# Kernel tuning notes

Hardware: AMD Instinct MI355X
Metric: run time of the kernel (lower is better)

Reference implementation:

```python
import jax, jax.numpy as jnp
import numpy as np

B, T, H, W = 64, 128, 64, 64
K = 3          # conv kernel size
NH = 64        # hidden_dim == n_qubits (required for the gating math to broadcast)
IN = 1         # input_dim (scalar conv feature per frame)
NC = 10        # num_classes


def setup_inputs() -> dict:
    key = jax.random.key(0)
    ks = jax.random.split(key, 32)
    i = iter(range(32))

    def lin(kw, kb, fan_in, fan_out):
        s = 1.0 / np.sqrt(fan_in)
        w = jax.random.uniform(kw, (fan_out, fan_in), jnp.float32, -s, s)
        b = jax.random.uniform(kb, (fan_out,), jnp.float32, -s, s)
        return w, b

    inp = {"images": jax.random.normal(ks[next(i)], (B, T, 1, H, W), jnp.float32)}
    inp["threshold"] = jnp.float32(0.5)
    s = 1.0 / np.sqrt(K * K)
    inp["conv_w"] = jax.random.uniform(ks[next(i)], (1, 1, K, K), jnp.float32, -s, s)
    inp["conv_b"] = jax.random.uniform(ks[next(i)], (1,), jnp.float32, -s, s)
    for g in ("f", "i", "u", "o"):
        w, b = lin(ks[next(i)], ks[next(i)], IN + NH, NH)
        inp[f"fc_{g}_w"], inp[f"fc_{g}_b"] = w, b
        lw, lb = lin(ks[next(i)], ks[next(i)], NH, NH)
        ew, eb = lin(ks[next(i)], ks[next(i)], NH, NH)
        inp[f"q_{g}_lw"], inp[f"q_{g}_lb"] = lw, lb
        inp[f"q_{g}_ew"], inp[f"q_{g}_eb"] = ew, eb
    inp["cls_w"], inp["cls_b"] = lin(ks[next(i)], ks[next(i)], NH, NC)
    return inp


def _qlayer(x, lw, lb, ew, eb):
    out = jnp.tanh(x @ lw.T + lb)
    return out * jax.nn.sigmoid(out @ ew.T + eb)


def reference(images, threshold, conv_w, conv_b,
              fc_f_w, fc_f_b, fc_i_w, fc_i_b, fc_u_w, fc_u_b, fc_o_w, fc_o_b,
              q_f_lw, q_f_lb, q_f_ew, q_f_eb,
              q_i_lw, q_i_lb, q_i_ew, q_i_eb,
              q_u_lw, q_u_lb, q_u_ew, q_u_eb,
              q_o_lw, q_o_lb, q_o_ew, q_o_eb,
              cls_w, cls_b):
    b, t, c, h, w = images.shape
    nh = q_f_lw.shape[0]
    # ConvFilter over all frames at once (vectorized across batch*time)
    x = images.reshape(b * t, c, h, w)
    logits = jax.lax.conv_general_dilated(
        x, conv_w, (1, 1), "VALID",
        dimension_numbers=("NCHW", "OIHW", "NCHW")) + conv_b[None, :, None, None]
    feat = jax.nn.sigmoid(logits - threshold).mean(axis=(2, 3))  # [B*T, 1]
    seq = feat.reshape(b, t, 1).transpose(1, 0, 2)               # [T, B, 1]

    def step(carry, xt):
        hx, cx = carry
        comb = jnp.concatenate([xt, hx], axis=1)                 # [B, 1+NH]
        f = jax.nn.sigmoid(_qlayer(comb @ fc_f_w.T + fc_f_b, q_f_lw, q_f_lb, q_f_ew, q_f_eb))
        i = jax.nn.sigmoid(_qlayer(comb @ fc_i_w.T + fc_i_b, q_i_lw, q_i_lb, q_i_ew, q_i_eb))
        g = jnp.tanh(_qlayer(comb @ fc_u_w.T + fc_u_b, q_u_lw, q_u_lb, q_u_ew, q_u_eb))
        o = jax.nn.sigmoid(_qlayer(comb @ fc_o_w.T + fc_o_b, q_o_lw, q_o_lb, q_o_ew, q_o_eb))
        cx = f * cx + i * g
        hx = o * jnp.tanh(cx)
        return (hx, cx), hx

    h0 = jnp.zeros((b, nh), images.dtype)
    c0 = jnp.zeros((b, nh), images.dtype)
    _, outs = jax.lax.scan(step, (h0, c0), seq)                  # [T, B, NH]
    return outs @ cls_w.T + cls_b                                # [T, B, NC]
```

## Files before the change

### kernel.cpp

```cpp
#include <hip/hip_runtime.h>

#define T_ 128
#define B_ 64
#define NH_ 64
#define NC_ 10

__device__ __forceinline__ float sigmoid_f(float x) {
    return 1.0f / (1.0f + __expf(-x));
}
__device__ __forceinline__ float tanh_f(float x) {
    return 1.0f - 2.0f / (1.0f + __expf(2.0f * x));
}
__device__ __forceinline__ void dot4(const float4 a, const float4 v,
                                     float& p0, float& p1, float& p2, float& p3) {
    p0 = fmaf(a.x, v.x, p0);
    p1 = fmaf(a.y, v.y, p1);
    p2 = fmaf(a.z, v.z, p2);
    p3 = fmaf(a.w, v.w, p3);
}

#define IMP 68
__global__ __launch_bounds__(256) void conv_feat(const float* __restrict__ img,
                                                 const float* __restrict__ cw,
                                                 const float* __restrict__ cb,
                                                 const float* __restrict__ thr,
                                                 float* __restrict__ feat) {
    __shared__ __align__(16) float im[64 * IMP];
    __shared__ float wsum[4];
    const int tid = threadIdx.x;
    const float* src = img + (size_t)blockIdx.x * 4096;
#pragma unroll
    for (int i = 0; i < 4; i++) {
        const int idx = i * 256 + tid;
        const int row = idx >> 4, c4 = idx & 15;
        *(float4*)&im[row * IMP + c4 * 4] = *(const float4*)&src[idx * 4];
    }
    const float w0 = cw[0], w1 = cw[1], w2 = cw[2], w3 = cw[3], w4 = cw[4],
                w5 = cw[5], w6 = cw[6], w7 = cw[7], w8 = cw[8];
    const float bias = cb[0] - thr[0];
    __syncthreads();

    const int r  = tid >> 2;
    const int c0 = (tid & 3) * 16;
    float sum = 0.0f;
    if (r < 62) {
        const int ncols = (c0 == 48) ? 14 : 16;
        float acc[16];
#pragma unroll
        for (int x = 0; x < 16; x++) acc[x] = bias;
#pragma unroll
        for (int dr = 0; dr < 3; dr++) {
            float rb[20];
#pragma unroll
            for (int j = 0; j < 5; j++) {
                float4 v = *(const float4*)&im[(r + dr) * IMP + c0 + j * 4];
                rb[j * 4 + 0] = v.x; rb[j * 4 + 1] = v.y;
                rb[j * 4 + 2] = v.z; rb[j * 4 + 3] = v.w;
            }
            const float k0 = (dr == 0) ? w0 : (dr == 1) ? w3 : w6;
            const float k1 = (dr == 0) ? w1 : (dr == 1) ? w4 : w7;
            const float k2 = (dr == 0) ? w2 : (dr == 1) ? w5 : w8;
#pragma unroll
            for (int x = 0; x < 16; x++) {
                acc[x] = fmaf(rb[x], k0, acc[x]);
                acc[x] = fmaf(rb[x + 1], k1, acc[x]);
                acc[x] = fmaf(rb[x + 2], k2, acc[x]);
            }
        }
#pragma unroll
        for (int x = 0; x < 16; x++)
            if (x < ncols) sum += sigmoid_f(acc[x]);
    }
#pragma unroll
    for (int off = 32; off >= 1; off >>= 1) sum += __shfl_down(sum, off, 64);
    const int wv = tid >> 6, ln = tid & 63;
    if (ln == 0) wsum[wv] = sum;
    __syncthreads();
    if (tid == 0)
        feat[blockIdx.x] = (wsum[0] + wsum[1] + wsum[2] + wsum[3]) * (1.0f / 3844.0f);
}

struct FuseArgs {
    const float* fcw[4];
    const float* fcb[4];
    const float* lw[4];
    const float* lb[4];
};

__global__ __launch_bounds__(256) void fuse_kernel(FuseArgs a, float* __restrict__ Aall,
                                                   float* __restrict__ Vall,
                                                   float* __restrict__ Call) {
    const int g = blockIdx.x;
    const float* fcw = a.fcw[g];
    const float* fcb = a.fcb[g];
    const float* lw  = a.lw[g];
    const float* lb  = a.lb[g];
    __shared__ float fcs[64 * 65];
    __shared__ float fbs[64];
    for (int i = threadIdx.x; i < 64 * 65; i += 256) fcs[i] = fcw[i];
    if (threadIdx.x < 64) fbs[threadIdx.x] = fcb[threadIdx.x];
    __syncthreads();

    const int n = threadIdx.x >> 2;
    const int j0 = (threadIdx.x & 3) * 16;
    float lrow[64];
#pragma unroll
    for (int k = 0; k < 64; k++) lrow[k] = lw[n * 64 + k];

    for (int j = j0; j < j0 + 16; j++) {
        float s = 0.0f;
#pragma unroll
        for (int k = 0; k < 64; k++) s = fmaf(lrow[k], fcs[k * 65 + j + 1], s);
        Aall[(g * 64 + n) * 64 + j] = s;
    }
    if ((threadIdx.x & 3) == 0) {
        float sv = 0.0f, sc = 0.0f;
#pragma unroll
        for (int k = 0; k < 64; k++) {
            sv = fmaf(lrow[k], fcs[k * 65], sv);
            sc = fmaf(lrow[k], fbs[k], sc);
        }
        Vall[g * 64 + n] = sv;
        Call[g * 64 + n] = sc + lb[n];
    }
}

__global__ __launch_bounds__(512, 1) void recur(
    const float* __restrict__ feat, const float* __restrict__ Aall,
    const float* __restrict__ Vall, const float* __restrict__ Call,
    const float* __restrict__ ew_f, const float* __restrict__ eb_f,
    const float* __restrict__ ew_i, const float* __restrict__ eb_i,
    const float* __restrict__ ew_u, const float* __restrict__ eb_u,
    const float* __restrict__ ew_o, const float* __restrict__ eb_o,
    const float* __restrict__ cls_w, const float* __restrict__ cls_b,
    float* __restrict__ out) {
    const int b = blockIdx.x;
    const int tid = threadIdx.x;
    const int wave = tid >> 6;
    const int g = wave >> 1;
    const int nh = wave & 1;
    const int lane = tid & 63;
    const int s = lane >> 5;
    const int n = nh * 32 + (lane & 31);
    const int gn = g * 64 + n;
    const float* ew  = (g == 0) ? ew_f : (g == 1) ? ew_i : (g == 2) ? ew_u : ew_o;
    const float* ebp = (g == 0) ? eb_f : (g == 1) ? eb_i : (g == 2) ? eb_u : eb_o;

    const float4* ap = (const float4*)&Aall[gn * 64 + s * 32];
    const float4* ep = (const float4*)&ew[n * 64 + s * 32];
    const float4 wa0 = ap[0], wa1 = ap[1], wa2 = ap[2], wa3 = ap[3];
    const float4 wa4 = ap[4], wa5 = ap[5], wa6 = ap[6], wa7 = ap[7];
    const float4 we0 = ep[0], we1 = ep[1], we2 = ep[2], we3 = ep[3];
    const float4 we4 = ep[4], we5 = ep[5], we6 = ep[6], we7 = ep[7];
    const float vj = Vall[gn], cj = Call[gn], ebj = ebp[n];

    __shared__ __align__(16) float hx[64];
    __shared__ __align__(16) float qsh[4][64];
    __shared__ __align__(16) float acts[2][4][64];
    __shared__ __align__(16) float xts[T_];
    __shared__ float hist[T_ * 65];
    __shared__ float cwts[NC_ * 65 + NC_];

    for (int i = tid; i < T_; i += 512) xts[i] = feat[b * T_ + i];
    for (int i = tid; i < NC_ * 64; i += 512) {
        int c = i >> 6, k = i & 63;
        cwts[c * 65 + k] = cls_w[i];
    }
    if (tid < NC_) cwts[NC_ * 65 + tid] = cls_b[tid];
    if (tid < 64) hx[tid] = 0.0f;
    float cx = 0.0f;
    __syncthreads();

    const float4* hp = (const float4*)&hx[s * 32];
    const float4* qp = (const float4*)&qsh[g][s * 32];

    for (int t = 0; t < T_; t++) {
        const float xt = xts[t];

        float p0 = 0, p1 = 0, p2 = 0, p3 = 0;
        {
            float4 v0 = hp[0], v1 = hp[1], v2 = hp[2], v3 = hp[3];
            float4 v4 = hp[4], v5 = hp[5], v6 = hp[6], v7 = hp[7];
            dot4(wa0, v0, p0, p1, p2, p3);
            dot4(wa1, v1, p0, p1, p2, p3);
            dot4(wa2, v2, p0, p1, p2, p3);
            dot4(wa3, v3, p0, p1, p2, p3);
            dot4(wa4, v4, p0, p1, p2, p3);
            dot4(wa5, v5, p0, p1, p2, p3);
            dot4(wa6, v6, p0, p1, p2, p3);
            dot4(wa7, v7, p0, p1, p2, p3);
        }
        float p = (p0 + p1) + (p2 + p3);
        p += __shfl_xor(p, 32, 64);
        const float q = tanh_f(fmaf(xt, vj, cj) + p);
        if (s == 0) qsh[g][n] = q;
        __syncthreads();

        p0 = 0; p1 = 0; p2 = 0; p3 = 0;
        {
            float4 v0 = qp[0], v1 = qp[1], v2 = qp[2], v3 = qp[3];
            float4 v4 = qp[4], v5 = qp[5], v6 = qp[6], v7 = qp[7];
            dot4(we0, v0, p0, p1, p2, p3);
            dot4(we1, v1, p0, p1, p2, p3);
            dot4(we2, v2, p0, p1, p2, p3);
            dot4(we3, v3, p0, p1, p2, p3);
            dot4(we4, v4, p0, p1, p2, p3);
            dot4(we5, v5, p0, p1, p2, p3);
            dot4(we6, v6, p0, p1, p2, p3);
            dot4(we7, v7, p0, p1, p2, p3);
        }
        p = (p0 + p1) + (p2 + p3);
        p += __shfl_xor(p, 32, 64);
        const float z = q * sigmoid_f(p + ebj);
        const float act = (g == 2) ? tanh_f(z) : sigmoid_f(z);
        if (s == 0) acts[t & 1][g][n] = act;
        __syncthreads();

        const float ff = acts[t & 1][0][n];
        const float ii = acts[t & 1][1][n];
        const float uu = acts[t & 1][2][n];
        const float oo = acts[t & 1][3][n];
        cx = fmaf(ff, cx, ii * uu);
        const float h = oo * tanh_f(cx);
        if (wave < 2 && s == 0) {
            hx[n] = h;
            hist[t * 65 + n] = h;
        }
        __syncthreads();
    }

#pragma unroll
    for (int j = 0; j < 3; j++) {
        const int o = j * 512 + tid;
        if (o < T_ * NC_) {
            const int r = o / 10;
            const int c = o - r * 10;
            float sacc = cwts[NC_ * 65 + c];
#pragma unroll 16
            for (int k = 0; k < 64; k++)
                sacc = fmaf(hist[r * 65 + k], cwts[c * 65 + k], sacc);
            out[((size_t)r * B_ + b) * NC_ + c] = sacc;
        }
    }
}

extern "C" void kernel_launch(void* const* d_in, const int* in_sizes, int n_in,
                              void* d_out, int out_size, void* d_ws, size_t ws_size,
                              hipStream_t stream) {
    const float* images = (const float*)d_in[0];
    const float* thr    = (const float*)d_in[1];
    const float* convw  = (const float*)d_in[2];
    const float* convb  = (const float*)d_in[3];
    const float* fcw[4]; const float* fcb[4]; const float* lw[4]; const float* lb[4];
    const float* ew[4];  const float* eb[4];
    for (int g = 0; g < 4; g++) {
        int base = 4 + g * 6;
        fcw[g] = (const float*)d_in[base + 0];
        fcb[g] = (const float*)d_in[base + 1];
        lw[g]  = (const float*)d_in[base + 2];
        lb[g]  = (const float*)d_in[base + 3];
        ew[g]  = (const float*)d_in[base + 4];
        eb[g]  = (const float*)d_in[base + 5];
    }
    const float* clsw = (const float*)d_in[28];
    const float* clsb = (const float*)d_in[29];

    float* ws   = (float*)d_ws;
    float* feat = ws;
    float* Aall = ws + 8192;
    float* Vall = ws + 24576;
    float* Call = ws + 24832;

    conv_feat<<<8192, 256, 0, stream>>>(images, convw, convb, thr, feat);

    FuseArgs fa;
    for (int g = 0; g < 4; g++) {
        fa.fcw[g] = fcw[g]; fa.fcb[g] = fcb[g];
        fa.lw[g] = lw[g];   fa.lb[g] = lb[g];
    }
    fuse_kernel<<<4, 256, 0, stream>>>(fa, Aall, Vall, Call);

    recur<<<B_, 512, 0, stream>>>(feat, Aall, Vall, Call,
                                  ew[0], eb[0], ew[1], eb[1],
                                  ew[2], eb[2], ew[3], eb[3],
                                  clsw, clsb, (float*)d_out);
}
```

Before: 163.5 us.

## Keep hidden state in registers and broadcast via ds_swizzle, dropping per-step barrier

Every wave now recomputes the full cell update in its own registers. Each lane owns one hidden unit, and the hidden vector reaches the first matvec through 32 ds_swizzle broadcasts. This removes the shared hx buffer and one of the three __syncthreads per timestep, cutting barrier latency on the serial recurrence's critical path. In exchange, the 8 vector LDS reads become 32 swizzle ops per step, and the cell math is repeated across all waves.

```diff
diff --git a/kernel.cpp b/kernel.cpp
--- a/kernel.cpp
+++ b/kernel.cpp
@@ -18,6 +18,10 @@
     p2 = fmaf(a.z, v.z, p2);
     p3 = fmaf(a.w, v.w, p3);
 }
+
+#define SWZF(J, WW, PP) { \
+    int swz_ = __builtin_amdgcn_ds_swizzle(h_bits, (J) << 5); \
+    PP = fmaf((WW), __int_as_float(swz_), PP); }
 
 #define IMP 68
 __global__ __launch_bounds__(256) void conv_feat(const float* __restrict__ img,
@@ -142,6 +146,7 @@
     const int lane = tid & 63;
     const int s = lane >> 5;
     const int n = nh * 32 + (lane & 31);
+    const int np = s * 32 + (lane & 31);
     const int gn = g * 64 + n;
     const float* ew  = (g == 0) ? ew_f : (g == 1) ? ew_i : (g == 2) ? ew_u : ew_o;
     const float* ebp = (g == 0) ? eb_f : (g == 1) ? eb_i : (g == 2) ? eb_u : eb_o;
@@ -154,7 +159,6 @@
     const float4 we4 = ep[4], we5 = ep[5], we6 = ep[6], we7 = ep[7];
     const float vj = Vall[gn], cj = Call[gn], ebj = ebp[n];
 
-    __shared__ __align__(16) float hx[64];
     __shared__ __align__(16) float qsh[4][64];
     __shared__ __align__(16) float acts[2][4][64];
     __shared__ __align__(16) float xts[T_];
@@ -167,29 +171,24 @@
         cwts[c * 65 + k] = cls_w[i];
     }
     if (tid < NC_) cwts[NC_ * 65 + tid] = cls_b[tid];
-    if (tid < 64) hx[tid] = 0.0f;
-    float cx = 0.0f;
-    __syncthreads();
-
-    const float4* hp = (const float4*)&hx[s * 32];
+    float cx = 0.0f, h_own = 0.0f;
+    __syncthreads();
+
     const float4* qp = (const float4*)&qsh[g][s * 32];
 
     for (int t = 0; t < T_; t++) {
         const float xt = xts[t];
 
+        const int h_bits = __float_as_int(h_own);
         float p0 = 0, p1 = 0, p2 = 0, p3 = 0;
-        {
-            float4 v0 = hp[0], v1 = hp[1], v2 = hp[2], v3 = hp[3];
-            float4 v4 = hp[4], v5 = hp[5], v6 = hp[6], v7 = hp[7];
-            dot4(wa0, v0, p0, p1, p2, p3);
-            dot4(wa1, v1, p0, p1, p2, p3);
-            dot4(wa2, v2, p0, p1, p2, p3);
-            dot4(wa3, v3, p0, p1, p2, p3);
-            dot4(wa4, v4, p0, p1, p2, p3);
-            dot4(wa5, v5, p0, p1, p2, p3);
-            dot4(wa6, v6, p0, p1, p2, p3);
-            dot4(wa7, v7, p0, p1, p2, p3);
-        }
+        SWZF(0,  wa0.x, p0) SWZF(1,  wa0.y, p1) SWZF(2,  wa0.z, p2) SWZF(3,  wa0.w, p3)
+        SWZF(4,  wa1.x, p0) SWZF(5,  wa1.y, p1) SWZF(6,  wa1.z, p2) SWZF(7,  wa1.w, p3)
+        SWZF(8,  wa2.x, p0) SWZF(9,  wa2.y, p1) SWZF(10, wa2.z, p2) SWZF(11, wa2.w, p3)
+        SWZF(12, wa3.x, p0) SWZF(13, wa3.y, p1) SWZF(14, wa3.z, p2) SWZF(15, wa3.w, p3)
+        SWZF(16, wa4.x, p0) SWZF(17, wa4.y, p1) SWZF(18, wa4.z, p2) SWZF(19, wa4.w, p3)
+        SWZF(20, wa5.x, p0) SWZF(21, wa5.y, p1) SWZF(22, wa5.z, p2) SWZF(23, wa5.w, p3)
+        SWZF(24, wa6.x, p0) SWZF(25, wa6.y, p1) SWZF(26, wa6.z, p2) SWZF(27, wa6.w, p3)
+        SWZF(28, wa7.x, p0) SWZF(29, wa7.y, p1) SWZF(30, wa7.z, p2) SWZF(31, wa7.w, p3)
         float p = (p0 + p1) + (p2 + p3);
         p += __shfl_xor(p, 32, 64);
         const float q = tanh_f(fmaf(xt, vj, cj) + p);
@@ -216,18 +215,15 @@
         if (s == 0) acts[t & 1][g][n] = act;
         __syncthreads();
 
-        const float ff = acts[t & 1][0][n];
-        const float ii = acts[t & 1][1][n];
-        const float uu = acts[t & 1][2][n];
-        const float oo = acts[t & 1][3][n];
+        const float ff = acts[t & 1][0][np];
+        const float ii = acts[t & 1][1][np];
+        const float uu = acts[t & 1][2][np];
+        const float oo = acts[t & 1][3][np];
         cx = fmaf(ff, cx, ii * uu);
-        const float h = oo * tanh_f(cx);
-        if (wave < 2 && s == 0) {
-            hx[n] = h;
-            hist[t * 65 + n] = h;
-        }
-        __syncthreads();
-    }
+        h_own = oo * tanh_f(cx);
+        if (wave == 0) hist[t * 65 + np] = h_own;
+    }
+    __syncthreads();
 
 #pragma unroll
     for (int j = 0; j < 3; j++) {
```

Measured after the change: 180.0 us. 1.1x slower.

## Drop per-step barrier in recurrence via per-wave hidden state; batch conv frames

Applied to the files above, without the earlier changes.

In the recurrence, every wave now redundantly computes the full 64-element cell/hidden update into its own private copy of the hidden state. This removes the second block-wide barrier per timestep, at the cost of duplicated elementwise work and extra shared memory. The conv kernel now processes four frames per block. It prefetches the next frame into registers while computing the current one, which cuts block count and overlaps global loads with compute.

```diff
diff --git a/kernel.cpp b/kernel.cpp
--- a/kernel.cpp
+++ b/kernel.cpp
@@ -20,6 +20,7 @@
 }
 
 #define IMP 68
+#define FPB 4
 __global__ __launch_bounds__(256) void conv_feat(const float* __restrict__ img,
                                                  const float* __restrict__ cw,
                                                  const float* __restrict__ cb,
@@ -28,56 +29,73 @@
     __shared__ __align__(16) float im[64 * IMP];
     __shared__ float wsum[4];
     const int tid = threadIdx.x;
-    const float* src = img + (size_t)blockIdx.x * 4096;
-#pragma unroll
-    for (int i = 0; i < 4; i++) {
-        const int idx = i * 256 + tid;
-        const int row = idx >> 4, c4 = idx & 15;
-        *(float4*)&im[row * IMP + c4 * 4] = *(const float4*)&src[idx * 4];
-    }
+    const float* base = img + (size_t)blockIdx.x * FPB * 4096;
     const float w0 = cw[0], w1 = cw[1], w2 = cw[2], w3 = cw[3], w4 = cw[4],
                 w5 = cw[5], w6 = cw[6], w7 = cw[7], w8 = cw[8];
     const float bias = cb[0] - thr[0];
-    __syncthreads();
-
+
+    const int rr = tid >> 4;
+    const int cc = (tid & 15) * 4;
     const int r  = tid >> 2;
     const int c0 = (tid & 3) * 16;
-    float sum = 0.0f;
-    if (r < 62) {
-        const int ncols = (c0 == 48) ? 14 : 16;
-        float acc[16];
-#pragma unroll
-        for (int x = 0; x < 16; x++) acc[x] = bias;
-#pragma unroll
-        for (int dr = 0; dr < 3; dr++) {
-            float rb[20];
-#pragma unroll
-            for (int j = 0; j < 5; j++) {
-                float4 v = *(const float4*)&im[(r + dr) * IMP + c0 + j * 4];
-                rb[j * 4 + 0] = v.x; rb[j * 4 + 1] = v.y;
-                rb[j * 4 + 2] = v.z; rb[j * 4 + 3] = v.w;
+    const int wv = tid >> 6, ln = tid & 63;
+
+    float4 pf0 = *(const float4*)&base[(0 * 256 + tid) * 4];
+    float4 pf1 = *(const float4*)&base[(1 * 256 + tid) * 4];
+    float4 pf2 = *(const float4*)&base[(2 * 256 + tid) * 4];
+    float4 pf3 = *(const float4*)&base[(3 * 256 + tid) * 4];
+
+    for (int f = 0; f < FPB; f++) {
+        *(float4*)&im[(0 * 16 + rr) * IMP + cc] = pf0;
+        *(float4*)&im[(1 * 16 + rr) * IMP + cc] = pf1;
+        *(float4*)&im[(2 * 16 + rr) * IMP + cc] = pf2;
+        *(float4*)&im[(3 * 16 + rr) * IMP + cc] = pf3;
+        if (f + 1 < FPB) {
+            const float* s = base + (size_t)(f + 1) * 4096;
+            pf0 = *(const float4*)&s[(0 * 256 + tid) * 4];
+            pf1 = *(const float4*)&s[(1 * 256 + tid) * 4];
+            pf2 = *(const float4*)&s[(2 * 256 + tid) * 4];
+            pf3 = *(const float4*)&s[(3 * 256 + tid) * 4];
+        }
+        __syncthreads();
+
+        float sum = 0.0f;
+        if (r < 62) {
+            const int ncols = (c0 == 48) ? 14 : 16;
+            float acc[16];
+#pragma unroll
+            for (int x = 0; x < 16; x++) acc[x] = bias;
+#pragma unroll
+            for (int dr = 0; dr < 3; dr++) {
+                float rb[20];
+#pragma unroll
+                for (int j = 0; j < 5; j++) {
+                    float4 v = *(const float4*)&im[(r + dr) * IMP + c0 + j * 4];
+                    rb[j * 4 + 0] = v.x; rb[j * 4 + 1] = v.y;
+                    rb[j * 4 + 2] = v.z; rb[j * 4 + 3] = v.w;
+                }
+                const float k0 = (dr == 0) ? w0 : (dr == 1) ? w3 : w6;
+                const float k1 = (dr == 0) ? w1 : (dr == 1) ? w4 : w7;
+                const float k2 = (dr == 0) ? w2 : (dr == 1) ? w5 : w8;
+#pragma unroll
+                for (int x = 0; x < 16; x++) {
+                    acc[x] = fmaf(rb[x], k0, acc[x]);
+                    acc[x] = fmaf(rb[x + 1], k1, acc[x]);
+                    acc[x] = fmaf(rb[x + 2], k2, acc[x]);
+                }
             }
-            const float k0 = (dr == 0) ? w0 : (dr == 1) ? w3 : w6;
-            const float k1 = (dr == 0) ? w1 : (dr == 1) ? w4 : w7;
-            const float k2 = (dr == 0) ? w2 : (dr == 1) ? w5 : w8;
-#pragma unroll
-            for (int x = 0; x < 16; x++) {
-                acc[x] = fmaf(rb[x], k0, acc[x]);
-                acc[x] = fmaf(rb[x + 1], k1, acc[x]);
-                acc[x] = fmaf(rb[x + 2], k2, acc[x]);
-            }
-        }
-#pragma unroll
-        for (int x = 0; x < 16; x++)
-            if (x < ncols) sum += sigmoid_f(acc[x]);
-    }
-#pragma unroll
-    for (int off = 32; off >= 1; off >>= 1) sum += __shfl_down(sum, off, 64);
-    const int wv = tid >> 6, ln = tid & 63;
-    if (ln == 0) wsum[wv] = sum;
-    __syncthreads();
-    if (tid == 0)
-        feat[blockIdx.x] = (wsum[0] + wsum[1] + wsum[2] + wsum[3]) * (1.0f / 3844.0f);
+#pragma unroll
+            for (int x = 0; x < 16; x++)
+                if (x < ncols) sum += sigmoid_f(acc[x]);
+        }
+#pragma unroll
+        for (int off = 32; off >= 1; off >>= 1) sum += __shfl_down(sum, off, 64);
+        if (ln == 0) wsum[wv] = sum;
+        __syncthreads();
+        if (tid == 0)
+            feat[blockIdx.x * FPB + f] =
+                (wsum[0] + wsum[1] + wsum[2] + wsum[3]) * (1.0f / 3844.0f);
+    }
 }
 
 struct FuseArgs {
@@ -142,6 +160,7 @@
     const int lane = tid & 63;
     const int s = lane >> 5;
     const int n = nh * 32 + (lane & 31);
+    const int np = s * 32 + (lane & 31);
     const int gn = g * 64 + n;
     const float* ew  = (g == 0) ? ew_f : (g == 1) ? ew_i : (g == 2) ? ew_u : ew_o;
     const float* ebp = (g == 0) ? eb_f : (g == 1) ? eb_i : (g == 2) ? eb_u : eb_o;
@@ -154,7 +173,7 @@
     const float4 we4 = ep[4], we5 = ep[5], we6 = ep[6], we7 = ep[7];
     const float vj = Vall[gn], cj = Call[gn], ebj = ebp[n];
 
-    __shared__ __align__(16) float hx[64];
+    __shared__ __align__(16) float hx8[8][64];
     __shared__ __align__(16) float qsh[4][64];
     __shared__ __align__(16) float acts[2][4][64];
     __shared__ __align__(16) float xts[T_];
@@ -167,11 +186,11 @@
         cwts[c * 65 + k] = cls_w[i];
     }
     if (tid < NC_) cwts[NC_ * 65 + tid] = cls_b[tid];
-    if (tid < 64) hx[tid] = 0.0f;
+    hx8[wave][lane] = 0.0f;
     float cx = 0.0f;
     __syncthreads();
 
-    const float4* hp = (const float4*)&hx[s * 32];
+    const float4* hp = (const float4*)&hx8[wave][s * 32];
     const float4* qp = (const float4*)&qsh[g][s * 32];
 
     for (int t = 0; t < T_; t++) {
@@ -216,18 +235,16 @@
         if (s == 0) acts[t & 1][g][n] = act;
         __syncthreads();
 
-        const float ff = acts[t & 1][0][n];
-        const float ii = acts[t & 1][1][n];
-        const float uu = acts[t & 1][2][n];
-        const float oo = acts[t & 1][3][n];
+        const float ff = acts[t & 1][0][np];
+        const float ii = acts[t & 1][1][np];
+        const float uu = acts[t & 1][2][np];
+        const float oo = acts[t & 1][3][np];
         cx = fmaf(ff, cx, ii * uu);
         const float h = oo * tanh_f(cx);
-        if (wave < 2 && s == 0) {
-            hx[n] = h;
-            hist[t * 65 + n] = h;
-        }
-        __syncthreads();
-    }
+        hx8[wave][np] = h;
+        if (wave == 0) hist[t * 65 + np] = h;
+    }
+    __syncthreads();
 
 #pragma unroll
     for (int j = 0; j < 3; j++) {
@@ -271,7 +288,7 @@
     float* Vall = ws + 24576;
     float* Call = ws + 24832;
 
-    conv_feat<<<8192, 256, 0, stream>>>(images, convw, convb, thr, feat);
+    conv_feat<<<8192 / FPB, 256, 0, stream>>>(images, convw, convb, thr, feat);
 
     FuseArgs fa;
     for (int g = 0; g < 4; g++) {
```

Result: no change. 163.3 us (-0.2%).
